# Optimization experiments

Measured on AMD Instinct MI355X. Metric: run time of the kernel, lower is better.

The kernel has to match this reference:

```python
import jax, jax.numpy as jnp
import numpy as np

B, S, D, H, F = 4, 1024, 512, 8, 2048
EPS = 1e-6


def _layernorm(x, g, b):
    m = jnp.mean(x, axis=-1, keepdims=True)
    v = jnp.mean(jnp.square(x - m), axis=-1, keepdims=True)
    return (x - m) * jax.lax.rsqrt(v + EPS) * g + b


def setup_inputs() -> dict:
    key = jax.random.key(0)
    ks = jax.random.split(key, 16)
    sd = 0.02
    return {
        "input_tensor": jax.random.normal(ks[0], (B, S, D), jnp.float32),
        # per-head QKV projections: each head maps D -> D (full depth, as in source)
        "Wq": jax.random.normal(ks[1], (H, D, D), jnp.float32) * sd,
        "bq": jnp.zeros((H, D), jnp.float32),
        "Wk": jax.random.normal(ks[2], (H, D, D), jnp.float32) * sd,
        "bk": jnp.zeros((H, D), jnp.float32),
        "Wv": jax.random.normal(ks[3], (H, D, D), jnp.float32) * sd,
        "bv": jnp.zeros((H, D), jnp.float32),
        # output projection after concat of H full-depth heads: (H*D) -> D
        "Wo": jax.random.normal(ks[4], (H * D, D), jnp.float32) * sd,
        "bo": jnp.zeros((D,), jnp.float32),
        "g1": jnp.ones((D,), jnp.float32),
        "beta1": jnp.zeros((D,), jnp.float32),
        "W1": jax.random.normal(ks[5], (D, F), jnp.float32) * sd,
        "b1": jnp.zeros((F,), jnp.float32),
        "W2": jax.random.normal(ks[6], (F, D), jnp.float32) * sd,
        "b2": jnp.zeros((D,), jnp.float32),
        "g2": jnp.ones((D,), jnp.float32),
        "beta2": jnp.zeros((D,), jnp.float32),
    }


def reference(input_tensor, Wq, bq, Wk, bk, Wv, bv, Wo, bo,
              g1, beta1, W1, b1, W2, b2, g2, beta2):
    x = input_tensor
    # batched per-head projections: [B,S,D] x [H,D,E] -> [B,H,S,E]
    q = jnp.einsum("bsd,hde->bhse", x, Wq) + bq[None, :, None, :]
    k = jnp.einsum("bsd,hde->bhse", x, Wk) + bk[None, :, None, :]
    v = jnp.einsum("bsd,hde->bhse", x, Wv) + bv[None, :, None, :]
    scale = 1.0 / jnp.sqrt(jnp.asarray(D, x.dtype))
    scores = jnp.einsum("bhse,bhte->bhst", q, k) * scale  # [B,H,S,S]
    attn = jax.nn.softmax(scores, axis=-1)
    heads = jnp.einsum("bhst,bhte->bhse", attn, v)  # [B,H,S,E]
    # concat heads on last axis: [B,S,H*D]
    concat = jnp.transpose(heads, (0, 2, 1, 3)).reshape(B, S, H * D)
    mha = concat @ Wo + bo  # [B,S,D]
    # dropout is identity at inference
    y = _layernorm(x + mha, g1, beta1)
    ff = jax.nn.relu(y @ W1 + b1) @ W2 + b2
    return _layernorm(y + ff, g2, beta2)
```

## Files before the change

kernel.cpp:

```cpp
#include <hip/hip_runtime.h>
#include <hip/hip_bf16.h>

typedef unsigned short u16;
typedef unsigned int u32;
typedef __attribute__((ext_vector_type(4))) float f32x4;
typedef __attribute__((ext_vector_type(8))) __bf16 bf16x8;

#define DEV __device__ __forceinline__

DEV u16 f2bf(float f) {
  union { float f; unsigned u; } c; c.f = f;
  unsigned r = (c.u + 0x7fffu + ((c.u >> 16) & 1u)) >> 16;
  return (u16)r;
}

DEV void gld_lds16(const void* g, void* l) {
  __builtin_amdgcn_global_load_lds(
      (__attribute__((address_space(1))) void*)g,
      (__attribute__((address_space(3))) void*)l, 16, 0, 0);
}

DEV f32x4 mfma_bf16(bf16x8 a, bf16x8 b, f32x4 c) {
  return __builtin_amdgcn_mfma_f32_16x16x32_bf16(a, b, c, 0, 0, 0);
}

DEV void bar_vm0() { asm volatile("s_waitcnt vmcnt(0) lgkmcnt(0)\n\ts_barrier" ::: "memory"); }
DEV void wait_lg0() { asm volatile("s_waitcnt lgkmcnt(0)" ::: "memory"); }

DEV u32 cvt_pk_bf16(float lo, float hi) {
  u32 d;
  asm("v_cvt_pk_bf16_f32 %0, %1, %2" : "=v"(d) : "v"(lo), "v"(hi));
  return d;
}

__global__ __launch_bounds__(256) void cvt_kernel(const float* __restrict__ in,
                                                  u16* __restrict__ out, int n4) {
  int i = blockIdx.x * 256 + threadIdx.x;
  if (i < n4) {
    float4 v = ((const float4*)in)[i];
    ushort4 o;
    o.x = f2bf(v.x); o.y = f2bf(v.y); o.z = f2bf(v.z); o.w = f2bf(v.w);
    ((ushort4*)out)[i] = o;
  }
}

__global__ __launch_bounds__(256) void transpose_cvt(const float* __restrict__ in,
                                                     u16* __restrict__ out, int R, int C) {
  __shared__ float t[32][33];
  size_t base = (size_t)blockIdx.z * R * C;
  const float* ip = in + base;
  u16* op = out + base;
  int c0 = blockIdx.x * 32, r0 = blockIdx.y * 32;
  int tx = threadIdx.x, ty = threadIdx.y;
#pragma unroll
  for (int i = 0; i < 4; ++i) {
    int rr = ty + i * 8;
    t[rr][tx] = ip[(size_t)(r0 + rr) * C + c0 + tx];
  }
  __syncthreads();
#pragma unroll
  for (int i = 0; i < 4; ++i) {
    int cc = ty + i * 8;
    op[(size_t)(c0 + cc) * R + r0 + tx] = f2bf(t[tx][cc]);
  }
}

template <int BM, int BN, int WM, int WN, int MODE>
__global__ __launch_bounds__(256) void gemm_tn(const u16* __restrict__ A,
                                               const u16* __restrict__ B, int N, int K,
                                               void* __restrict__ out0, void* __restrict__ out1,
                                               const float* __restrict__ bias0,
                                               const float* __restrict__ bias1) {
  constexpr int BK = 64;
  constexpr int MF = WM / 16, NF = WN / 16;
  constexpr int WC = BN / WN;
  constexpr int AI = (BM * BK / 8) / 256;
  constexpr int BI = (BN * BK / 8) / 256;
  __shared__ u16 As[2][BM * BK];
  __shared__ u16 Bs[2][BN * BK];
  const int tid = threadIdx.x;
  const int wave = tid >> 6, lane = tid & 63;
  const int r = lane & 15, g = lane >> 4;
  const int row0 = blockIdx.y * BM, col0 = blockIdx.x * BN;
  const int wr = (wave / WC) * WM, wc = (wave % WC) * WN;

  auto stage = [&](int kt, int p) {
#pragma unroll
    for (int i = 0; i < AI; ++i) {
      int c = i * 256 + wave * 64 + lane;
      int row = c >> 3, ch = (c & 7) ^ (row & 7);
      gld_lds16(A + (size_t)(row0 + row) * K + kt + ch * 8,
                &As[p][(size_t)(i * 256 + wave * 64) * 8]);
    }
#pragma unroll
    for (int i = 0; i < BI; ++i) {
      int c = i * 256 + wave * 64 + lane;
      int row = c >> 3, ch = (c & 7) ^ (row & 7);
      gld_lds16(B + (size_t)(col0 + row) * K + kt + ch * 8,
                &Bs[p][(size_t)(i * 256 + wave * 64) * 8]);
    }
  };

  f32x4 acc[MF][NF] = {};
  const int nt = K / BK;

  stage(0, 0);
  for (int t = 0; t < nt; ++t) {
    const int p = t & 1;
    bar_vm0();
    if (t + 1 < nt) stage((t + 1) * BK, p ^ 1);
    __builtin_amdgcn_s_setprio(1);
#pragma unroll
    for (int kk = 0; kk < 2; ++kk) {
      bf16x8 af[MF], bfv[NF];
#pragma unroll
      for (int m = 0; m < MF; ++m)
        af[m] = *(const bf16x8*)(&As[p][(wr + m * 16 + r) * BK + (((kk * 4 + g) ^ (r & 7))) * 8]);
#pragma unroll
      for (int n = 0; n < NF; ++n)
        bfv[n] = *(const bf16x8*)(&Bs[p][(wc + n * 16 + r) * BK + (((kk * 4 + g) ^ (r & 7))) * 8]);
#pragma unroll
      for (int m = 0; m < MF; ++m)
#pragma unroll
        for (int n = 0; n < NF; ++n)
          acc[m][n] = mfma_bf16(af[m], bfv[n], acc[m][n]);
    }
    __builtin_amdgcn_s_setprio(0);
  }

#pragma unroll
  for (int m = 0; m < MF; ++m) {
#pragma unroll
    for (int n = 0; n < NF; ++n) {
      int gcol = col0 + wc + n * 16 + r;
#pragma unroll
      for (int j = 0; j < 4; ++j) {
        int grow = row0 + wr + m * 16 + g * 4 + j;
        float val = acc[m][n][j];
        if constexpr (MODE == 0) {
          int p = gcol >> 12;
          int he = gcol & 4095;
          u16* dst = (u16*)(p ? out1 : out0);
          const float* bsp = p ? bias1 : bias0;
          val += bsp[he];
          int bb = grow >> 10, s = grow & 1023;
          size_t off = (((size_t)(bb * 8 + (he >> 9)) * 1024 + s) * 512) + (he & 511);
          dst[off] = f2bf(val);
        } else if constexpr (MODE == 1) {
          val += bias0[grow];
          int bb = gcol >> 10, s = gcol & 1023;
          size_t off = (((size_t)bb * 8 + (grow >> 9)) * 512 + (grow & 511)) * 1024 + s;
          ((u16*)out0)[off] = f2bf(val);
        } else if constexpr (MODE == 2) {
          ((float*)out0)[(size_t)grow * N + gcol] = val + bias0[gcol];
        } else {
          float v2 = fmaxf(val + bias0[gcol], 0.0f);
          ((u16*)out0)[(size_t)grow * N + gcol] = f2bf(v2);
        }
      }
    }
  }
  (void)out1; (void)bias1;
}

__global__ __launch_bounds__(512, 2) void flash_kernel(const u16* __restrict__ qg,
                                                       const u16* __restrict__ kg,
                                                       const u16* __restrict__ vtg,
                                                       u16* __restrict__ concat) {
  constexpr float SCALE = 0.04419417382415922f;
  __shared__ u16 Ks[2][32 * 512];
  __shared__ u16 Vs[2][32 * 512];
  __shared__ u32 PsU[8][256];

  const int tid = threadIdx.x;
  const int wave = tid >> 6, lane = tid & 63;
  const int r = lane & 15, g = lane >> 4;
  const int bx = blockIdx.x;
  const int xcd = bx & 7, slot = bx >> 3;
  const int bh = xcd * 4 + (slot >> 3);
  const int qt = slot & 7;
  const int bb = bh >> 3, hh = bh & 7;
  const size_t hbase = (size_t)bh * 1024 * 512;
  const u16* qp = qg + hbase;
  const u16* kp = kg + hbase;
  const u16* vp = vtg + hbase;
  const int q0 = qt * 128;

  bf16x8 q[16];
#pragma unroll
  for (int kk = 0; kk < 16; ++kk)
    q[kk] = *(const bf16x8*)(qp + (size_t)(q0 + wave * 16 + r) * 512 + kk * 32 + g * 8);

  const int krow8 = lane >> 3, kch = (lane & 7) ^ (lane >> 3);
  const int vrow4 = lane >> 2, vch = (lane & 3) ^ ((lane >> 2) & 3);
  auto stageKV = [&](int t, int p) {
    int kv = t * 32;
#pragma unroll
    for (int j = 0; j < 4; ++j) {
      int id = wave * 4 + j;
      gld_lds16(kp + (size_t)(kv + j * 8 + krow8) * 512 + wave * 64 + kch * 8,
                &Ks[p][id * 512]);
    }
#pragma unroll
    for (int j = 0; j < 4; ++j) {
      int n = wave * 4 + j;
      gld_lds16(vp + (size_t)(n * 16 + vrow4) * 1024 + kv + vch * 8, &Vs[p][n * 512]);
    }
  };

  f32x4 o[32] = {};
  float mrun = -1e30f, lrun = 0.f;

  stageKV(0, 0);

  const int krh = (r >> 3) * 512;
  const int ke0 = (r & 7) * 64 + ((g ^ (r & 7)) * 8);
  const int ke1 = (r & 7) * 64 + (((4 + g) ^ (r & 7)) * 8);
  const int voff = (r * 4 + (g ^ (r & 3))) * 8;

  for (int t = 0; t < 32; ++t) {
    const int p = t & 1;
    bar_vm0();
    if (t < 31) stageKV(t + 1, p ^ 1);

    __builtin_amdgcn_s_setprio(1);
    f32x4 a0 = {}, a1 = {}, b0 = {}, b1 = {};
#pragma unroll
    for (int kc = 0; kc < 8; ++kc) {
      const u16* kb = &Ks[p][kc * 2048 + krh];
      bf16x8 kf00 = *(const bf16x8*)(kb + ke0);
      bf16x8 kf01 = *(const bf16x8*)(kb + 1024 + ke0);
      bf16x8 kf10 = *(const bf16x8*)(kb + ke1);
      bf16x8 kf11 = *(const bf16x8*)(kb + 1024 + ke1);
      a0 = mfma_bf16(kf00, q[2 * kc], a0);
      b0 = mfma_bf16(kf01, q[2 * kc], b0);
      a1 = mfma_bf16(kf10, q[2 * kc + 1], a1);
      b1 = mfma_bf16(kf11, q[2 * kc + 1], b1);
    }
    __builtin_amdgcn_s_setprio(0);
    f32x4 s0 = a0 + a1;
    f32x4 s1 = b0 + b1;

    float m8 = -1e30f;
#pragma unroll
    for (int j = 0; j < 4; ++j) {
      s0[j] *= SCALE;
      s1[j] *= SCALE;
      m8 = fmaxf(m8, fmaxf(s0[j], s1[j]));
    }
    m8 = fmaxf(m8, __shfl_xor(m8, 16));
    m8 = fmaxf(m8, __shfl_xor(m8, 32));
    if (__any(m8 - mrun > 6.0f)) {
      float mn = fmaxf(mrun, m8);
      float rs = __expf(mrun - mn);
      mrun = mn;
      lrun *= rs;
#pragma unroll
      for (int j = 0; j < 4; ++j) {
        float rsj = __shfl(rs, (lane & 48) | (g * 4 + j));
#pragma unroll
        for (int n = 0; n < 32; ++n) o[n][j] *= rsj;
      }
    }
    f32x4 p0, p1;
    float ls = 0.f;
#pragma unroll
    for (int j = 0; j < 4; ++j) {
      p0[j] = __expf(s0[j] - mrun);
      p1[j] = __expf(s1[j] - mrun);
      ls += p0[j] + p1[j];
    }
    ls += __shfl_xor(ls, 16);
    ls += __shfl_xor(ls, 32);
    lrun += ls;

    {
      u32* pw = &PsU[wave][0];
      int base = r * 4 + (g & 1) * 2 + (g >> 1) * 64;
      pw[base + 0] = cvt_pk_bf16(p0[0], p0[1]);
      pw[base + 1] = cvt_pk_bf16(p0[2], p0[3]);
      pw[base + 128 + 0] = cvt_pk_bf16(p1[0], p1[1]);
      pw[base + 128 + 1] = cvt_pk_bf16(p1[2], p1[3]);
    }
    wait_lg0();

    bf16x8 pa = *(const bf16x8*)&PsU[wave][lane * 4];
    __builtin_amdgcn_s_setprio(1);
#pragma unroll
    for (int n = 0; n < 32; ++n) {
      bf16x8 bv = *(const bf16x8*)&Vs[p][n * 512 + voff];
      o[n] = mfma_bf16(pa, bv, o[n]);
    }
    __builtin_amdgcn_s_setprio(0);
  }

  float invl = 1.0f / lrun;
#pragma unroll
  for (int j = 0; j < 4; ++j) {
    float inv = __shfl(invl, (lane & 48) | (g * 4 + j));
    int srow = q0 + wave * 16 + g * 4 + j;
    size_t rowoff = ((size_t)bb * 1024 + srow) * 4096;
#pragma unroll
    for (int n = 0; n < 32; ++n) {
      int ocol = hh * 512 + n * 16 + r;
      concat[rowoff + ocol] = f2bf(o[n][j] * inv);
    }
  }
}

__global__ __launch_bounds__(128) void add_ln_kernel(const float* __restrict__ xin,
                                                     const float* __restrict__ addin,
                                                     const float* __restrict__ gamma,
                                                     const float* __restrict__ beta,
                                                     float* __restrict__ yout,
                                                     u16* __restrict__ ybout) {
  int row = blockIdx.x;
  int t = threadIdx.x;
  float4 xv = ((const float4*)(xin + (size_t)row * 512))[t];
  float4 av = ((const float4*)(addin + (size_t)row * 512))[t];
  float v0 = xv.x + av.x, v1 = xv.y + av.y, v2 = xv.z + av.z, v3 = xv.w + av.w;
  float s1 = v0 + v1 + v2 + v3;
  float s2 = v0 * v0 + v1 * v1 + v2 * v2 + v3 * v3;
#pragma unroll
  for (int d = 1; d < 64; d <<= 1) {
    s1 += __shfl_xor(s1, d);
    s2 += __shfl_xor(s2, d);
  }
  __shared__ float sh[4];
  int wv = t >> 6;
  if ((t & 63) == 0) { sh[wv * 2] = s1; sh[wv * 2 + 1] = s2; }
  __syncthreads();
  s1 = sh[0] + sh[2];
  s2 = sh[1] + sh[3];
  float mean = s1 * (1.0f / 512.0f);
  float var = s2 * (1.0f / 512.0f) - mean * mean;
  float rstd = rsqrtf(var + 1e-6f);
  float4 gv = ((const float4*)gamma)[t];
  float4 bv = ((const float4*)beta)[t];
  float o0 = (v0 - mean) * rstd * gv.x + bv.x;
  float o1 = (v1 - mean) * rstd * gv.y + bv.y;
  float o2 = (v2 - mean) * rstd * gv.z + bv.z;
  float o3 = (v3 - mean) * rstd * gv.w + bv.w;
  float4 ov; ov.x = o0; ov.y = o1; ov.z = o2; ov.w = o3;
  ((float4*)(yout + (size_t)row * 512))[t] = ov;
  if (ybout) {
    ushort4 ub;
    ub.x = f2bf(o0); ub.y = f2bf(o1); ub.z = f2bf(o2); ub.w = f2bf(o3);
    ((ushort4*)(ybout + (size_t)row * 512))[t] = ub;
  }
}

extern "C" void kernel_launch(void* const* d_in, const int* in_sizes, int n_in, void* d_out,
                              int out_size, void* d_ws, size_t ws_size, hipStream_t stream) {
  (void)in_sizes; (void)n_in; (void)out_size; (void)ws_size;
  const float* x   = (const float*)d_in[0];
  const float* Wq  = (const float*)d_in[1];
  const float* bq  = (const float*)d_in[2];
  const float* Wk  = (const float*)d_in[3];
  const float* bk  = (const float*)d_in[4];
  const float* Wv  = (const float*)d_in[5];
  const float* bv  = (const float*)d_in[6];
  const float* Wo  = (const float*)d_in[7];
  const float* bo  = (const float*)d_in[8];
  const float* g1  = (const float*)d_in[9];
  const float* be1 = (const float*)d_in[10];
  const float* W1  = (const float*)d_in[11];
  const float* b1  = (const float*)d_in[12];
  const float* W2  = (const float*)d_in[13];
  const float* b2  = (const float*)d_in[14];
  const float* g2  = (const float*)d_in[15];
  const float* be2 = (const float*)d_in[16];

  char* ws = (char*)d_ws;
  const size_t MB = 1024 * 1024;
  u16*   xb   = (u16*)(ws + 0);
  u16*   wqkT = (u16*)(ws + 4 * MB);
  u16*   wvT  = (u16*)(ws + 12 * MB);
  u16*   woT  = (u16*)(ws + 16 * MB);
  u16*   w1T  = (u16*)(ws + 20 * MB);
  u16*   w2T  = (u16*)(ws + 22 * MB);
  u16*   qb   = (u16*)(ws + 24 * MB);
  u16*   kb   = (u16*)(ws + 56 * MB);
  u16*   vTb  = (u16*)(ws + 88 * MB);
  u16*   cc   = (u16*)(ws + 120 * MB);
  float* mha  = (float*)(ws + 24 * MB);
  float* y    = (float*)(ws + 32 * MB);
  u16*   yb   = (u16*)(ws + 40 * MB);
  u16*   ff1  = (u16*)(ws + 56 * MB);
  float* ff2  = (float*)(ws + 72 * MB);

  cvt_kernel<<<2048, 256, 0, stream>>>(x, xb, 524288);
  transpose_cvt<<<dim3(16, 16, 8), dim3(32, 8), 0, stream>>>(Wq, wqkT, 512, 512);
  transpose_cvt<<<dim3(16, 16, 8), dim3(32, 8), 0, stream>>>(Wk, wqkT + 8 * 512 * 512, 512, 512);
  transpose_cvt<<<dim3(16, 16, 8), dim3(32, 8), 0, stream>>>(Wv, wvT, 512, 512);
  transpose_cvt<<<dim3(16, 128, 1), dim3(32, 8), 0, stream>>>(Wo, woT, 4096, 512);
  transpose_cvt<<<dim3(64, 16, 1), dim3(32, 8), 0, stream>>>(W1, w1T, 512, 2048);
  transpose_cvt<<<dim3(16, 64, 1), dim3(32, 8), 0, stream>>>(W2, w2T, 2048, 512);

  gemm_tn<128, 128, 64, 64, 0><<<dim3(64, 32), 256, 0, stream>>>(xb, wqkT, 8192, 512, qb, kb, bq, bk);
  gemm_tn<128, 128, 64, 64, 1><<<dim3(32, 32), 256, 0, stream>>>(wvT, xb, 4096, 512, vTb, nullptr, bv, nullptr);
  flash_kernel<<<256, 512, 0, stream>>>(qb, kb, vTb, cc);
  gemm_tn<64, 128, 32, 64, 2><<<dim3(4, 64), 256, 0, stream>>>(cc, woT, 512, 4096, mha, nullptr, bo, nullptr);
  add_ln_kernel<<<4096, 128, 0, stream>>>(x, mha, g1, be1, y, yb);
  gemm_tn<128, 128, 64, 64, 3><<<dim3(16, 32), 256, 0, stream>>>(yb, w1T, 2048, 512, ff1, nullptr, b1, nullptr);
  gemm_tn<64, 128, 32, 64, 2><<<dim3(4, 64), 256, 0, stream>>>(ff1, w2T, 512, 2048, ff2, nullptr, b2, nullptr);
  add_ln_kernel<<<4096, 128, 0, stream>>>(y, ff2, g2, be2, (float*)d_out, nullptr);
}
```

Measured before the change: 307.7 us.

## Fuse prep launches into one kernel and enlarge QKV GEMM tiles to 256x256

Merges the bf16 conversion of x and the six weight transpose-conversions into a single prep kernel that dispatches on block index, which removes six kernel launches. The GEMM template gains a thread-count parameter, and the Q/K and V projections now use 512-thread blocks with 256x256 tiles to get more operand reuse per block, at the cost of fewer blocks and higher LDS use. The flash kernel's V-tile swizzle pattern is also changed to alter LDS bank mapping. The swizzle edit has to stay consistent between the store and load sides to remain correct.

```diff
diff --git a/kernel.cpp b/kernel.cpp
--- a/kernel.cpp
+++ b/kernel.cpp
@@ -33,29 +33,63 @@
   return d;
 }
 
-__global__ __launch_bounds__(256) void cvt_kernel(const float* __restrict__ in,
-                                                  u16* __restrict__ out, int n4) {
-  int i = blockIdx.x * 256 + threadIdx.x;
-  if (i < n4) {
-    float4 v = ((const float4*)in)[i];
+__global__ __launch_bounds__(256) void prep_kernel(const float* __restrict__ x,
+                                                   const float* __restrict__ Wq,
+                                                   const float* __restrict__ Wk,
+                                                   const float* __restrict__ Wv,
+                                                   const float* __restrict__ Wo,
+                                                   const float* __restrict__ W1,
+                                                   const float* __restrict__ W2,
+                                                   u16* __restrict__ xb, u16* __restrict__ wqT,
+                                                   u16* __restrict__ wkT, u16* __restrict__ wvT,
+                                                   u16* __restrict__ woT, u16* __restrict__ w1T,
+                                                   u16* __restrict__ w2T) {
+  int b = blockIdx.x;
+  int tid = threadIdx.x;
+  if (b < 2048) {
+    int i = b * 256 + tid;
+    float4 v = ((const float4*)x)[i];
     ushort4 o;
     o.x = f2bf(v.x); o.y = f2bf(v.y); o.z = f2bf(v.z); o.w = f2bf(v.w);
-    ((ushort4*)out)[i] = o;
-  }
-}
-
-__global__ __launch_bounds__(256) void transpose_cvt(const float* __restrict__ in,
-                                                     u16* __restrict__ out, int R, int C) {
+    ((ushort4*)xb)[i] = o;
+    return;
+  }
+  int idx = b - 2048;
+  const float* in;
+  u16* out;
+  int R, C, bx, by, bz = 0;
+  if (idx < 6144) {
+    int job = idx >> 11;
+    in = job == 0 ? Wq : (job == 1 ? Wk : Wv);
+    out = job == 0 ? wqT : (job == 1 ? wkT : wvT);
+    int rr = idx & 2047;
+    bz = rr >> 8;
+    by = (rr >> 4) & 15;
+    bx = rr & 15;
+    R = 512; C = 512;
+  } else if (idx < 8192) {
+    int rr = idx - 6144;
+    in = Wo; out = woT; R = 4096; C = 512;
+    by = rr >> 4; bx = rr & 15;
+  } else if (idx < 9216) {
+    int rr = idx - 8192;
+    in = W1; out = w1T; R = 512; C = 2048;
+    by = rr >> 6; bx = rr & 63;
+  } else {
+    int rr = idx - 9216;
+    in = W2; out = w2T; R = 2048; C = 512;
+    by = rr >> 4; bx = rr & 15;
+  }
   __shared__ float t[32][33];
-  size_t base = (size_t)blockIdx.z * R * C;
+  size_t base = (size_t)bz * R * C;
   const float* ip = in + base;
   u16* op = out + base;
-  int c0 = blockIdx.x * 32, r0 = blockIdx.y * 32;
-  int tx = threadIdx.x, ty = threadIdx.y;
+  int c0 = bx * 32, r0 = by * 32;
+  int tx = tid & 31, ty = tid >> 5;
 #pragma unroll
   for (int i = 0; i < 4; ++i) {
-    int rr = ty + i * 8;
-    t[rr][tx] = ip[(size_t)(r0 + rr) * C + c0 + tx];
+    int rr2 = ty + i * 8;
+    t[rr2][tx] = ip[(size_t)(r0 + rr2) * C + c0 + tx];
   }
   __syncthreads();
 #pragma unroll
@@ -65,17 +99,17 @@
   }
 }
 
-template <int BM, int BN, int WM, int WN, int MODE>
-__global__ __launch_bounds__(256) void gemm_tn(const u16* __restrict__ A,
-                                               const u16* __restrict__ B, int N, int K,
-                                               void* __restrict__ out0, void* __restrict__ out1,
-                                               const float* __restrict__ bias0,
-                                               const float* __restrict__ bias1) {
+template <int NT, int BM, int BN, int WM, int WN, int MODE>
+__global__ __launch_bounds__(NT) void gemm_tn(const u16* __restrict__ A,
+                                              const u16* __restrict__ B, int N, int K,
+                                              void* __restrict__ out0, void* __restrict__ out1,
+                                              const float* __restrict__ bias0,
+                                              const float* __restrict__ bias1) {
   constexpr int BK = 64;
   constexpr int MF = WM / 16, NF = WN / 16;
   constexpr int WC = BN / WN;
-  constexpr int AI = (BM * BK / 8) / 256;
-  constexpr int BI = (BN * BK / 8) / 256;
+  constexpr int AI = (BM * BK / 8) / NT;
+  constexpr int BI = (BN * BK / 8) / NT;
   __shared__ u16 As[2][BM * BK];
   __shared__ u16 Bs[2][BN * BK];
   const int tid = threadIdx.x;
@@ -87,17 +121,17 @@
   auto stage = [&](int kt, int p) {
 #pragma unroll
     for (int i = 0; i < AI; ++i) {
-      int c = i * 256 + wave * 64 + lane;
+      int bi = i * NT + wave * 64;
+      int c = bi + lane;
       int row = c >> 3, ch = (c & 7) ^ (row & 7);
-      gld_lds16(A + (size_t)(row0 + row) * K + kt + ch * 8,
-                &As[p][(size_t)(i * 256 + wave * 64) * 8]);
+      gld_lds16(A + (size_t)(row0 + row) * K + kt + ch * 8, &As[p][(size_t)bi * 8]);
     }
 #pragma unroll
     for (int i = 0; i < BI; ++i) {
-      int c = i * 256 + wave * 64 + lane;
+      int bi = i * NT + wave * 64;
+      int c = bi + lane;
       int row = c >> 3, ch = (c & 7) ^ (row & 7);
-      gld_lds16(B + (size_t)(col0 + row) * K + kt + ch * 8,
-                &Bs[p][(size_t)(i * 256 + wave * 64) * 8]);
+      gld_lds16(B + (size_t)(col0 + row) * K + kt + ch * 8, &Bs[p][(size_t)bi * 8]);
     }
   };
 
@@ -138,10 +172,10 @@
         int grow = row0 + wr + m * 16 + g * 4 + j;
         float val = acc[m][n][j];
         if constexpr (MODE == 0) {
-          int p = gcol >> 12;
+          int ph = gcol >> 12;
           int he = gcol & 4095;
-          u16* dst = (u16*)(p ? out1 : out0);
-          const float* bsp = p ? bias1 : bias0;
+          u16* dst = (u16*)(ph ? out1 : out0);
+          const float* bsp = ph ? bias1 : bias0;
           val += bsp[he];
           int bb = grow >> 10, s = grow & 1023;
           size_t off = (((size_t)(bb * 8 + (he >> 9)) * 1024 + s) * 512) + (he & 511);
@@ -192,7 +226,7 @@
     q[kk] = *(const bf16x8*)(qp + (size_t)(q0 + wave * 16 + r) * 512 + kk * 32 + g * 8);
 
   const int krow8 = lane >> 3, kch = (lane & 7) ^ (lane >> 3);
-  const int vrow4 = lane >> 2, vch = (lane & 3) ^ ((lane >> 2) & 3);
+  const int vrow4 = lane >> 2, vch = (lane & 3) ^ ((lane >> 3) & 3);
   auto stageKV = [&](int t, int p) {
     int kv = t * 32;
 #pragma unroll
@@ -216,7 +250,7 @@
   const int krh = (r >> 3) * 512;
   const int ke0 = (r & 7) * 64 + ((g ^ (r & 7)) * 8);
   const int ke1 = (r & 7) * 64 + (((4 + g) ^ (r & 7)) * 8);
-  const int voff = (r * 4 + (g ^ (r & 3))) * 8;
+  const int voff = (r * 4 + (g ^ ((r >> 1) & 3))) * 8;
 
   for (int t = 0; t < 32; ++t) {
     const int p = t & 1;
@@ -389,20 +423,15 @@
   u16*   ff1  = (u16*)(ws + 56 * MB);
   float* ff2  = (float*)(ws + 72 * MB);
 
-  cvt_kernel<<<2048, 256, 0, stream>>>(x, xb, 524288);
-  transpose_cvt<<<dim3(16, 16, 8), dim3(32, 8), 0, stream>>>(Wq, wqkT, 512, 512);
-  transpose_cvt<<<dim3(16, 16, 8), dim3(32, 8), 0, stream>>>(Wk, wqkT + 8 * 512 * 512, 512, 512);
-  transpose_cvt<<<dim3(16, 16, 8), dim3(32, 8), 0, stream>>>(Wv, wvT, 512, 512);
-  transpose_cvt<<<dim3(16, 128, 1), dim3(32, 8), 0, stream>>>(Wo, woT, 4096, 512);
-  transpose_cvt<<<dim3(64, 16, 1), dim3(32, 8), 0, stream>>>(W1, w1T, 512, 2048);
-  transpose_cvt<<<dim3(16, 64, 1), dim3(32, 8), 0, stream>>>(W2, w2T, 2048, 512);
-
-  gemm_tn<128, 128, 64, 64, 0><<<dim3(64, 32), 256, 0, stream>>>(xb, wqkT, 8192, 512, qb, kb, bq, bk);
-  gemm_tn<128, 128, 64, 64, 1><<<dim3(32, 32), 256, 0, stream>>>(wvT, xb, 4096, 512, vTb, nullptr, bv, nullptr);
+  prep_kernel<<<12288, 256, 0, stream>>>(x, Wq, Wk, Wv, Wo, W1, W2, xb, wqkT,
+                                         wqkT + 8 * 512 * 512, wvT, woT, w1T, w2T);
+
+  gemm_tn<512, 256, 256, 128, 64, 0><<<dim3(32, 16), 512, 0, stream>>>(xb, wqkT, 8192, 512, qb, kb, bq, bk);
+  gemm_tn<512, 256, 256, 128, 64, 1><<<dim3(16, 16), 512, 0, stream>>>(wvT, xb, 4096, 512, vTb, nullptr, bv, nullptr);
   flash_kernel<<<256, 512, 0, stream>>>(qb, kb, vTb, cc);
-  gemm_tn<64, 128, 32, 64, 2><<<dim3(4, 64), 256, 0, stream>>>(cc, woT, 512, 4096, mha, nullptr, bo, nullptr);
+  gemm_tn<256, 64, 128, 32, 64, 2><<<dim3(4, 64), 256, 0, stream>>>(cc, woT, 512, 4096, mha, nullptr, bo, nullptr);
   add_ln_kernel<<<4096, 128, 0, stream>>>(x, mha, g1, be1, y, yb);
-  gemm_tn<128, 128, 64, 64, 3><<<dim3(16, 32), 256, 0, stream>>>(yb, w1T, 2048, 512, ff1, nullptr, b1, nullptr);
-  gemm_tn<64, 128, 32, 64, 2><<<dim3(4, 64), 256, 0, stream>>>(ff1, w2T, 512, 2048, ff2, nullptr, b2, nullptr);
+  gemm_tn<256, 128, 128, 64, 64, 3><<<dim3(16, 32), 256, 0, stream>>>(yb, w1T, 2048, 512, ff1, nullptr, b1, nullptr);
+  gemm_tn<256, 64, 128, 32, 64, 2><<<dim3(4, 64), 256, 0, stream>>>(ff1, w2T, 512, 2048, ff2, nullptr, b2, nullptr);
   add_ln_kernel<<<4096, 128, 0, stream>>>(y, ff2, g2, be2, (float*)d_out, nullptr);
 }
```

Result: faster. 293.9 us (-4.5%).
